# Performance work log

Hardware: AMD Instinct MI355X
Metric: run time of the kernel (lower is better)

The kernel has to match this reference:

```python
import jax, jax.numpy as jnp
import numpy as np

UNITS = 128
FILTERS = 32
KSIZE = 31
B, T, DV, DQ = 64, 1000, 512, 1024


def setup_inputs() -> dict:
    key = jax.random.key(0)
    ks = jax.random.split(key, 12)
    scale = 0.05
    inp = {
        "query": jax.random.normal(ks[0], (B, DQ), jnp.float32),
        "values": jax.random.normal(ks[1], (B, T, DV), jnp.float32),
        "previous_attention_weights": jax.random.uniform(ks[2], (B, T, 1), jnp.float32),
        # learned params
        "Wq": jax.random.normal(ks[3], (DQ, UNITS), jnp.float32) * scale,
        "bq": jnp.zeros((UNITS,), jnp.float32),
        "Wm": jax.random.normal(ks[4], (DV, UNITS), jnp.float32) * scale,
        "bm": jnp.zeros((UNITS,), jnp.float32),
        "Wv": jax.random.normal(ks[5], (UNITS, 1), jnp.float32) * scale,
        "bv": jnp.zeros((1,), jnp.float32),
        "Wconv": jax.random.normal(ks[6], (KSIZE, 1, FILTERS), jnp.float32) * scale,  # [W, Cin, Cout]
        "Wl": jax.random.normal(ks[7], (FILTERS, UNITS), jnp.float32) * scale,
    }
    return inp


def _forward(query, values, prev_w, Wq, bq, Wm, bm, Wv, bv, Wconv, Wl):
    # location features: Conv1D (same padding, no bias) then Dense(tanh, no bias)
    loc = jax.lax.conv_general_dilated(
        prev_w, Wconv, window_strides=(1,), padding="SAME",
        dimension_numbers=("NWC", "WIO", "NWC"))          # [B, T, FILTERS]
    loc = jnp.tanh(loc @ Wl)                                # [B, T, UNITS]
    q = query @ Wq + bq                                     # [B, UNITS]
    m = values @ Wm + bm                                    # [B, T, UNITS]
    score = jnp.tanh(m + q[:, None, :] + loc) @ Wv + bv     # [B, T, 1]
    attention_weights = jax.nn.softmax(score, axis=1)       # softmax over time
    context = jnp.sum(attention_weights * values, axis=1)   # [B, DV]
    return context, attention_weights


def reference(query, values, previous_attention_weights, Wq, bq, Wm, bm, Wv, bv, Wconv, Wl):
    return _forward(query, values, previous_attention_weights,
                    Wq, bq, Wm, bm, Wv, bv, Wconv, Wl)
```

## Files before the change

kernel.cpp:

```cpp
#include <hip/hip_runtime.h>

#define B_  64
#define T_  1000
#define DV_ 512
#define DQ_ 1024
#define U_  128
#define F_  32
#define KS_ 31
#define P_  8

typedef __attribute__((ext_vector_type(8))) short short8;
typedef __attribute__((ext_vector_type(4))) float f32x4;

__device__ __forceinline__ unsigned pk2(float a, float b) {
    union { float f; unsigned u; } x, y;
    x.f = a; y.f = b;
    unsigned ra = (x.u + 0x7FFFu + ((x.u >> 16) & 1u)) >> 16;
    unsigned rb = (y.u + 0x7FFFu + ((y.u >> 16) & 1u)) >> 16;
    return (ra & 0xFFFFu) | (rb << 16);
}

__device__ __forceinline__ float fast_tanh(float x) {
    return 1.0f - 2.0f / (__expf(2.0f * x) + 1.0f);
}

__device__ __forceinline__ short8 loadA8(const float* __restrict__ p) {
    float4 f0 = *(const float4*)p;
    float4 f1 = *(const float4*)(p + 4);
    int4 q;
    q.x = pk2(f0.x, f0.y); q.y = pk2(f0.z, f0.w);
    q.z = pk2(f1.x, f1.y); q.w = pk2(f1.z, f1.w);
    return *(short8*)&q;
}

__global__ void prep_kernel(const float* __restrict__ Wm, const float* __restrict__ Wl,
                            short* __restrict__ WmX, short* __restrict__ WlX) {
    int g = blockIdx.x * 256 + threadIdx.x;
    if (g < 8192) {
        int kc = g >> 9, e = g & 511;
        int n = e >> 2, q = e & 3;
        int kb = kc * 32 + q * 8;
        int4 p;
        p.x = pk2(Wm[(kb + 0) * U_ + n], Wm[(kb + 1) * U_ + n]);
        p.y = pk2(Wm[(kb + 2) * U_ + n], Wm[(kb + 3) * U_ + n]);
        p.z = pk2(Wm[(kb + 4) * U_ + n], Wm[(kb + 5) * U_ + n]);
        p.w = pk2(Wm[(kb + 6) * U_ + n], Wm[(kb + 7) * U_ + n]);
        ((int4*)WmX)[g] = p;
    } else if (g < 8704) {
        int e = g - 8192;
        int n = e >> 2, q = e & 3;
        int kb = q * 8;
        int4 p;
        p.x = pk2(Wl[(kb + 0) * U_ + n], Wl[(kb + 1) * U_ + n]);
        p.y = pk2(Wl[(kb + 2) * U_ + n], Wl[(kb + 3) * U_ + n]);
        p.z = pk2(Wl[(kb + 4) * U_ + n], Wl[(kb + 5) * U_ + n]);
        p.w = pk2(Wl[(kb + 6) * U_ + n], Wl[(kb + 7) * U_ + n]);
        ((int4*)WlX)[e] = p;
    }
}

__global__ __launch_bounds__(1024) void qb_kernel(
    const float* __restrict__ query, const float* __restrict__ Wq,
    const float* __restrict__ bq, const float* __restrict__ bm,
    float* __restrict__ qb)
{
    __shared__ float qs[DQ_];
    __shared__ float red[8][U_];
    int b = blockIdx.x, tid = threadIdx.x;
    qs[tid] = query[b * DQ_ + tid];
    __syncthreads();
    int u = tid & 127, p = tid >> 7;
    float a = 0.f;
    const float* wp = Wq + (size_t)p * 128 * U_ + u;
    const float* qp = qs + p * 128;
#pragma unroll 8
    for (int k = 0; k < 128; ++k) a += qp[k] * wp[(size_t)k * U_];
    red[p][u] = a;
    __syncthreads();
    if (tid < U_) {
        float s = bq[tid] + bm[tid];
#pragma unroll
        for (int pp = 0; pp < 8; ++pp) s += red[pp][tid];
        qb[b * U_ + tid] = s;
    }
}

__global__ __launch_bounds__(256) void score_kernel(
    const float* __restrict__ values, const float* __restrict__ prev,
    const float* __restrict__ Wc, const float* __restrict__ Wv,
    const float* __restrict__ bv, const short* __restrict__ WmX,
    const short* __restrict__ WlX, const float* __restrict__ qb,
    float* __restrict__ scores)
{
    __shared__ float WcS[KS_ * F_];
    __shared__ short AsL[2048];
    __shared__ float qbS[2 * U_];
    __shared__ float WvS[U_];

    const int tid = threadIdx.x;
    const int r0 = blockIdx.x * 64;
    const int b0 = r0 / T_;
    const int b1 = (r0 + 63) / T_;

    for (int i = tid; i < KS_ * F_; i += 256) WcS[i] = Wc[i];
    if (tid < U_) WvS[tid] = Wv[tid];
    {
        int bb = (tid < U_) ? b0 : b1;
        qbS[tid] = qb[bb * U_ + (tid & (U_ - 1))];
    }

    const int wv = tid >> 6, lane = tid & 63;
    const int quad = lane >> 4, m15 = lane & 15;
    const int row = wv * 16 + m15;
    const float* aP = values + (size_t)(r0 + row) * DV_ + quad * 8;
    const int4* bW  = (const int4*)WmX + m15 * 4 + quad;
    const int4* blW = (const int4*)WlX + m15 * 4 + quad;

    short8 afA, afB;
    int4 bfA[8], bfB[8];
    afA = loadA8(aP);
#pragma unroll
    for (int c = 0; c < 8; ++c) bfA[c] = bW[c * 64];

    __syncthreads();

    {
        int i = lane, fg = wv;
        int r = r0 + i;
        int b = r / T_;
        int t = r - b * T_;
        const float* pv = prev + b * T_;
        float a8[8] = {};
#pragma unroll
        for (int k = 0; k < KS_; ++k) {
            int tt = t + k - 15;
            float p = ((unsigned)tt < (unsigned)T_) ? pv[tt] : 0.f;
#pragma unroll
            for (int j = 0; j < 8; ++j) a8[j] += p * WcS[k * F_ + fg * 8 + j];
        }
        int4 pq;
        pq.x = pk2(a8[0], a8[1]); pq.y = pk2(a8[2], a8[3]);
        pq.z = pk2(a8[4], a8[5]); pq.w = pk2(a8[6], a8[7]);
        ((int4*)AsL)[i * 4 + (fg ^ ((i >> 1) & 3))] = pq;
    }
    __syncthreads();

    f32x4 acc[8];
    {
        short8 afl = ((const short8*)AsL)[row * 4 + (quad ^ ((row >> 1) & 3))];
        f32x4 lacc[8] = {};
#pragma unroll
        for (int c = 0; c < 8; ++c) {
            int4 bl = blW[c * 64];
            lacc[c] = __builtin_amdgcn_mfma_f32_16x16x32_bf16(afl, *(short8*)&bl, lacc[c], 0, 0, 0);
        }
        int qoff[4];
#pragma unroll
        for (int v = 0; v < 4; ++v) {
            int r = r0 + wv * 16 + quad * 4 + v;
            qoff[v] = ((r / T_) == b0) ? 0 : U_;
        }
#pragma unroll
        for (int c = 0; c < 8; ++c) {
            int col = c * 16 + m15;
#pragma unroll
            for (int v = 0; v < 4; ++v)
                acc[c][v] = qbS[qoff[v] + col] + fast_tanh(lacc[c][v]);
        }
    }

#pragma unroll
    for (int k2 = 0; k2 < 8; ++k2) {
        const int kc = k2 * 2;
        afB = loadA8(aP + (kc + 1) * 32);
#pragma unroll
        for (int c = 0; c < 8; ++c) bfB[c] = bW[(kc + 1) * 512 + c * 64];
#pragma unroll
        for (int c = 0; c < 8; ++c)
            acc[c] = __builtin_amdgcn_mfma_f32_16x16x32_bf16(afA, *(short8*)&bfA[c], acc[c], 0, 0, 0);
        if (kc + 2 < 16) {
            afA = loadA8(aP + (kc + 2) * 32);
#pragma unroll
            for (int c = 0; c < 8; ++c) bfA[c] = bW[(kc + 2) * 512 + c * 64];
        }
#pragma unroll
        for (int c = 0; c < 8; ++c)
            acc[c] = __builtin_amdgcn_mfma_f32_16x16x32_bf16(afB, *(short8*)&bfB[c], acc[c], 0, 0, 0);
    }

    float psum[4] = {0.f, 0.f, 0.f, 0.f};
#pragma unroll
    for (int c = 0; c < 8; ++c) {
        int col = c * 16 + m15;
        float wvv = WvS[col];
#pragma unroll
        for (int v = 0; v < 4; ++v)
            psum[v] += fast_tanh(acc[c][v]) * wvv;
    }
#pragma unroll
    for (int off = 1; off < 16; off <<= 1) {
#pragma unroll
        for (int v = 0; v < 4; ++v) psum[v] += __shfl_xor(psum[v], off);
    }
    if (m15 == 0) {
        float bvv = bv[0];
#pragma unroll
        for (int v = 0; v < 4; ++v)
            scores[r0 + wv * 16 + quad * 4 + v] = psum[v] + bvv;
    }
}

__global__ void softmax_kernel(const float* __restrict__ s, float* __restrict__ w) {
    __shared__ float red[4];
    int b = blockIdx.x, tid = threadIdx.x;
    const float* sb = s + b * T_;
    float v[4];
    int tv[4];
#pragma unroll
    for (int i = 0; i < 4; ++i) {
        int t = tid + i * 256;
        tv[i] = t;
        v[i] = (t < T_) ? sb[t] : -1e30f;
    }
    float mx = fmaxf(fmaxf(v[0], v[1]), fmaxf(v[2], v[3]));
#pragma unroll
    for (int off = 32; off >= 1; off >>= 1) mx = fmaxf(mx, __shfl_xor(mx, off));
    int wv = tid >> 6, lane = tid & 63;
    if (lane == 0) red[wv] = mx;
    __syncthreads();
    mx = fmaxf(fmaxf(red[0], red[1]), fmaxf(red[2], red[3]));
    float e[4];
    float sum = 0.f;
#pragma unroll
    for (int i = 0; i < 4; ++i) {
        e[i] = (tv[i] < T_) ? __expf(v[i] - mx) : 0.f;
        sum += e[i];
    }
#pragma unroll
    for (int off = 32; off >= 1; off >>= 1) sum += __shfl_xor(sum, off);
    __syncthreads();
    if (lane == 0) red[wv] = sum;
    __syncthreads();
    sum = red[0] + red[1] + red[2] + red[3];
    float inv = 1.0f / sum;
#pragma unroll
    for (int i = 0; i < 4; ++i)
        if (tv[i] < T_) w[b * T_ + tv[i]] = e[i] * inv;
}

__global__ __launch_bounds__(256) void ctx1_kernel(
    const float* __restrict__ values, const float* __restrict__ w,
    float* __restrict__ part)
{
    __shared__ float wS[125];
    int b = blockIdx.x, p = blockIdx.y, tid = threadIdx.x;
    if (tid < 125) wS[tid] = w[b * T_ + p * 125 + tid];
    __syncthreads();
    const float* vp = values + ((size_t)b * T_ + p * 125) * DV_ + tid * 2;
    float ax = 0.f, ay = 0.f;
#pragma unroll 5
    for (int t = 0; t < 125; ++t) {
        float2 v = *(const float2*)(vp + (size_t)t * DV_);
        ax += wS[t] * v.x;
        ay += wS[t] * v.y;
    }
    float2 o; o.x = ax; o.y = ay;
    *(float2*)(part + ((size_t)(b * P_ + p)) * DV_ + tid * 2) = o;
}

__global__ void ctx2_kernel(const float* __restrict__ part, float* __restrict__ ctx) {
    int b = blockIdx.x, tid = threadIdx.x;
    float ax = 0.f, ay = 0.f;
    const float* pp = part + (size_t)b * P_ * DV_ + tid * 2;
#pragma unroll
    for (int p = 0; p < P_; ++p) {
        float2 v = *(const float2*)(pp + (size_t)p * DV_);
        ax += v.x; ay += v.y;
    }
    float2 o; o.x = ax; o.y = ay;
    *(float2*)(ctx + (size_t)b * DV_ + tid * 2) = o;
}

extern "C" void kernel_launch(void* const* d_in, const int* in_sizes, int n_in,
                              void* d_out, int out_size, void* d_ws, size_t ws_size,
                              hipStream_t stream) {
    const float* query  = (const float*)d_in[0];
    const float* values = (const float*)d_in[1];
    const float* prev   = (const float*)d_in[2];
    const float* Wq     = (const float*)d_in[3];
    const float* bq     = (const float*)d_in[4];
    const float* Wm     = (const float*)d_in[5];
    const float* bm     = (const float*)d_in[6];
    const float* Wv     = (const float*)d_in[7];
    const float* bv     = (const float*)d_in[8];
    const float* Wc     = (const float*)d_in[9];
    const float* Wl     = (const float*)d_in[10];

    float* out  = (float*)d_out;
    float* ctx  = out;
    float* attw = out + B_ * DV_;

    char* ws = (char*)d_ws;
    float* qb     = (float*)(ws);
    float* scores = (float*)(ws + 32768);
    short* WmX    = (short*)(ws + 32768 + 256000);
    short* WlX    = (short*)(ws + 32768 + 256000 + 131072);
    float* part   = (float*)(ws + 32768 + 256000 + 131072 + 8192);

    prep_kernel<<<34, 256, 0, stream>>>(Wm, Wl, WmX, WlX);
    qb_kernel<<<B_, 1024, 0, stream>>>(query, Wq, bq, bm, qb);
    score_kernel<<<1000, 256, 0, stream>>>(values, prev, Wc, Wv, bv, WmX, WlX, qb, scores);
    softmax_kernel<<<B_, 256, 0, stream>>>(scores, attw);
    ctx1_kernel<<<dim3(B_, P_), 256, 0, stream>>>(values, attw, part);
    ctx2_kernel<<<B_, 256, 0, stream>>>(part, ctx);
}
```

Measured before the change: 273.6 us.

## Merge prep and qb kernels, double score tile rows, widen ctx partitions

Prep and qb kernels are merged into one launch. The score kernel now processes 128 rows per block with two MFMA row groups sharing each weight fragment, which halves the B-operand traffic per row, and it uses a three-stage register prefetch of activations. The context reduction is split into 16 time chunks using float4 loads and an in-block two-way reduction, and ctx2 is vectorized. These changes raise register pressure in the score kernel and leave only 500 blocks to fill the device.

```diff
diff --git a/kernel.cpp b/kernel.cpp
--- a/kernel.cpp
+++ b/kernel.cpp
@@ -7,7 +7,8 @@
 #define U_  128
 #define F_  32
 #define KS_ 31
-#define P_  8
+#define P_  16
+#define CT_ 63
 
 typedef __attribute__((ext_vector_type(8))) short short8;
 typedef __attribute__((ext_vector_type(4))) float f32x4;
@@ -24,64 +25,64 @@
     return 1.0f - 2.0f / (__expf(2.0f * x) + 1.0f);
 }
 
-__device__ __forceinline__ short8 loadA8(const float* __restrict__ p) {
-    float4 f0 = *(const float4*)p;
-    float4 f1 = *(const float4*)(p + 4);
+__device__ __forceinline__ short8 pk8(float4 f0, float4 f1) {
     int4 q;
     q.x = pk2(f0.x, f0.y); q.y = pk2(f0.z, f0.w);
     q.z = pk2(f1.x, f1.y); q.w = pk2(f1.z, f1.w);
     return *(short8*)&q;
 }
 
-__global__ void prep_kernel(const float* __restrict__ Wm, const float* __restrict__ Wl,
-                            short* __restrict__ WmX, short* __restrict__ WlX) {
-    int g = blockIdx.x * 256 + threadIdx.x;
-    if (g < 8192) {
-        int kc = g >> 9, e = g & 511;
-        int n = e >> 2, q = e & 3;
-        int kb = kc * 32 + q * 8;
-        int4 p;
-        p.x = pk2(Wm[(kb + 0) * U_ + n], Wm[(kb + 1) * U_ + n]);
-        p.y = pk2(Wm[(kb + 2) * U_ + n], Wm[(kb + 3) * U_ + n]);
-        p.z = pk2(Wm[(kb + 4) * U_ + n], Wm[(kb + 5) * U_ + n]);
-        p.w = pk2(Wm[(kb + 6) * U_ + n], Wm[(kb + 7) * U_ + n]);
-        ((int4*)WmX)[g] = p;
-    } else if (g < 8704) {
-        int e = g - 8192;
-        int n = e >> 2, q = e & 3;
-        int kb = q * 8;
-        int4 p;
-        p.x = pk2(Wl[(kb + 0) * U_ + n], Wl[(kb + 1) * U_ + n]);
-        p.y = pk2(Wl[(kb + 2) * U_ + n], Wl[(kb + 3) * U_ + n]);
-        p.z = pk2(Wl[(kb + 4) * U_ + n], Wl[(kb + 5) * U_ + n]);
-        p.w = pk2(Wl[(kb + 6) * U_ + n], Wl[(kb + 7) * U_ + n]);
-        ((int4*)WlX)[e] = p;
-    }
-}
-
-__global__ __launch_bounds__(1024) void qb_kernel(
+__global__ __launch_bounds__(1024) void prep_qb_kernel(
+    const float* __restrict__ Wm, const float* __restrict__ Wl,
     const float* __restrict__ query, const float* __restrict__ Wq,
     const float* __restrict__ bq, const float* __restrict__ bm,
-    float* __restrict__ qb)
+    short* __restrict__ WmX, short* __restrict__ WlX, float* __restrict__ qb)
 {
-    __shared__ float qs[DQ_];
-    __shared__ float red[8][U_];
-    int b = blockIdx.x, tid = threadIdx.x;
-    qs[tid] = query[b * DQ_ + tid];
-    __syncthreads();
-    int u = tid & 127, p = tid >> 7;
-    float a = 0.f;
-    const float* wp = Wq + (size_t)p * 128 * U_ + u;
-    const float* qp = qs + p * 128;
+    __shared__ float sh[DQ_ + 8 * U_];
+    int blk = blockIdx.x, tid = threadIdx.x;
+    if (blk < 9) {
+        int g = blk * 1024 + tid;
+        if (g < 8192) {
+            int kc = g >> 9, e = g & 511;
+            int n = e >> 2, q = e & 3;
+            int kb = kc * 32 + q * 8;
+            int4 p;
+            p.x = pk2(Wm[(kb + 0) * U_ + n], Wm[(kb + 1) * U_ + n]);
+            p.y = pk2(Wm[(kb + 2) * U_ + n], Wm[(kb + 3) * U_ + n]);
+            p.z = pk2(Wm[(kb + 4) * U_ + n], Wm[(kb + 5) * U_ + n]);
+            p.w = pk2(Wm[(kb + 6) * U_ + n], Wm[(kb + 7) * U_ + n]);
+            ((int4*)WmX)[g] = p;
+        } else if (g < 8704) {
+            int e = g - 8192;
+            int n = e >> 2, q = e & 3;
+            int kb = q * 8;
+            int4 p;
+            p.x = pk2(Wl[(kb + 0) * U_ + n], Wl[(kb + 1) * U_ + n]);
+            p.y = pk2(Wl[(kb + 2) * U_ + n], Wl[(kb + 3) * U_ + n]);
+            p.z = pk2(Wl[(kb + 4) * U_ + n], Wl[(kb + 5) * U_ + n]);
+            p.w = pk2(Wl[(kb + 6) * U_ + n], Wl[(kb + 7) * U_ + n]);
+            ((int4*)WlX)[e] = p;
+        }
+    } else {
+        float* qs = sh;
+        float* red = sh + DQ_;
+        int b = blk - 9;
+        qs[tid] = query[b * DQ_ + tid];
+        __syncthreads();
+        int u = tid & 127, p = tid >> 7;
+        float a = 0.f;
+        const float* wp = Wq + (size_t)p * 128 * U_ + u;
+        const float* qp = qs + p * 128;
 #pragma unroll 8
-    for (int k = 0; k < 128; ++k) a += qp[k] * wp[(size_t)k * U_];
-    red[p][u] = a;
-    __syncthreads();
-    if (tid < U_) {
-        float s = bq[tid] + bm[tid];
-#pragma unroll
-        for (int pp = 0; pp < 8; ++pp) s += red[pp][tid];
-        qb[b * U_ + tid] = s;
+        for (int k = 0; k < 128; ++k) a += qp[k] * wp[(size_t)k * U_];
+        red[p * U_ + u] = a;
+        __syncthreads();
+        if (tid < U_) {
+            float s = bq[tid] + bm[tid];
+#pragma unroll
+            for (int pp = 0; pp < 8; ++pp) s += red[pp * U_ + tid];
+            qb[b * U_ + tid] = s;
+        }
     }
 }
 
@@ -93,14 +94,14 @@
     float* __restrict__ scores)
 {
     __shared__ float WcS[KS_ * F_];
-    __shared__ short AsL[2048];
+    __shared__ short AsL[128 * 32];
     __shared__ float qbS[2 * U_];
     __shared__ float WvS[U_];
 
     const int tid = threadIdx.x;
-    const int r0 = blockIdx.x * 64;
+    const int r0 = blockIdx.x * 128;
     const int b0 = r0 / T_;
-    const int b1 = (r0 + 63) / T_;
+    const int b1 = (r0 + 127) / T_;
 
     for (int i = tid; i < KS_ * F_; i += 256) WcS[i] = Wc[i];
     if (tid < U_) WvS[tid] = Wv[tid];
@@ -111,21 +112,27 @@
 
     const int wv = tid >> 6, lane = tid & 63;
     const int quad = lane >> 4, m15 = lane & 15;
-    const int row = wv * 16 + m15;
-    const float* aP = values + (size_t)(r0 + row) * DV_ + quad * 8;
+    const int row0 = wv * 32 + m15;
+    const float* aP0 = values + (size_t)(r0 + row0) * DV_ + quad * 8;
+    const float* aP1 = aP0 + (size_t)16 * DV_;
     const int4* bW  = (const int4*)WmX + m15 * 4 + quad;
     const int4* blW = (const int4*)WlX + m15 * 4 + quad;
 
-    short8 afA, afB;
-    int4 bfA[8], bfB[8];
-    afA = loadA8(aP);
-#pragma unroll
-    for (int c = 0; c < 8; ++c) bfA[c] = bW[c * 64];
-
-    __syncthreads();
-
-    {
-        int i = lane, fg = wv;
+    float4 aq0[2][2], aq1[2][2], aq2[2][2];
+    int4 bf0[8], bf1[8];
+    aq0[0][0] = *(const float4*)(aP0);      aq0[0][1] = *(const float4*)(aP0 + 4);
+    aq0[1][0] = *(const float4*)(aP1);      aq0[1][1] = *(const float4*)(aP1 + 4);
+    aq1[0][0] = *(const float4*)(aP0 + 32); aq1[0][1] = *(const float4*)(aP0 + 36);
+    aq1[1][0] = *(const float4*)(aP1 + 32); aq1[1][1] = *(const float4*)(aP1 + 36);
+#pragma unroll
+    for (int c = 0; c < 8; ++c) bf0[c] = bW[c * 64];
+
+    __syncthreads();
+
+#pragma unroll
+    for (int it = 0; it < 2; ++it) {
+        int idx = tid + it * 256;
+        int i = idx & 127, fg = idx >> 7;
         int r = r0 + i;
         int b = r / T_;
         int t = r - b * T_;
@@ -145,68 +152,89 @@
     }
     __syncthreads();
 
-    f32x4 acc[8];
+    f32x4 acc[2][8] = {};
     {
-        short8 afl = ((const short8*)AsL)[row * 4 + (quad ^ ((row >> 1) & 3))];
-        f32x4 lacc[8] = {};
+        int row1 = row0 + 16;
+        short8 afl0 = ((const short8*)AsL)[row0 * 4 + (quad ^ ((row0 >> 1) & 3))];
+        short8 afl1 = ((const short8*)AsL)[row1 * 4 + (quad ^ ((row1 >> 1) & 3))];
 #pragma unroll
         for (int c = 0; c < 8; ++c) {
             int4 bl = blW[c * 64];
-            lacc[c] = __builtin_amdgcn_mfma_f32_16x16x32_bf16(afl, *(short8*)&bl, lacc[c], 0, 0, 0);
-        }
-        int qoff[4];
-#pragma unroll
-        for (int v = 0; v < 4; ++v) {
-            int r = r0 + wv * 16 + quad * 4 + v;
-            qoff[v] = ((r / T_) == b0) ? 0 : U_;
-        }
+            acc[0][c] = __builtin_amdgcn_mfma_f32_16x16x32_bf16(afl0, *(short8*)&bl, acc[0][c], 0, 0, 0);
+            acc[1][c] = __builtin_amdgcn_mfma_f32_16x16x32_bf16(afl1, *(short8*)&bl, acc[1][c], 0, 0, 0);
+        }
+        int qoff[2][4];
+#pragma unroll
+        for (int g = 0; g < 2; ++g)
+#pragma unroll
+            for (int v = 0; v < 4; ++v) {
+                int r = r0 + wv * 32 + g * 16 + quad * 4 + v;
+                qoff[g][v] = ((r / T_) == b0) ? 0 : U_;
+            }
+#pragma unroll
+        for (int g = 0; g < 2; ++g)
+#pragma unroll
+            for (int c = 0; c < 8; ++c) {
+                int col = c * 16 + m15;
+#pragma unroll
+                for (int v = 0; v < 4; ++v)
+                    acc[g][c][v] = qbS[qoff[g][v] + col] + fast_tanh(acc[g][c][v]);
+            }
+    }
+
+#pragma unroll
+    for (int kc = 0; kc < 16; ++kc) {
+        if (kc + 2 < 16) {
+            aq2[0][0] = *(const float4*)(aP0 + (kc + 2) * 32);
+            aq2[0][1] = *(const float4*)(aP0 + (kc + 2) * 32 + 4);
+            aq2[1][0] = *(const float4*)(aP1 + (kc + 2) * 32);
+            aq2[1][1] = *(const float4*)(aP1 + (kc + 2) * 32 + 4);
+        }
+        if (kc + 1 < 16) {
+#pragma unroll
+            for (int c = 0; c < 8; ++c) bf1[c] = bW[(kc + 1) * 512 + c * 64];
+        }
+        short8 af0 = pk8(aq0[0][0], aq0[0][1]);
+        short8 af1 = pk8(aq0[1][0], aq0[1][1]);
+#pragma unroll
+        for (int c = 0; c < 8; ++c) {
+            acc[0][c] = __builtin_amdgcn_mfma_f32_16x16x32_bf16(af0, *(short8*)&bf0[c], acc[0][c], 0, 0, 0);
+            acc[1][c] = __builtin_amdgcn_mfma_f32_16x16x32_bf16(af1, *(short8*)&bf0[c], acc[1][c], 0, 0, 0);
+        }
+#pragma unroll
+        for (int g = 0; g < 2; ++g) {
+            aq0[g][0] = aq1[g][0]; aq0[g][1] = aq1[g][1];
+            aq1[g][0] = aq2[g][0]; aq1[g][1] = aq2[g][1];
+        }
+#pragma unroll
+        for (int c = 0; c < 8; ++c) bf0[c] = bf1[c];
+    }
+
+    float psum[2][4] = {};
+#pragma unroll
+    for (int g = 0; g < 2; ++g)
 #pragma unroll
         for (int c = 0; c < 8; ++c) {
             int col = c * 16 + m15;
+            float wvv = WvS[col];
 #pragma unroll
             for (int v = 0; v < 4; ++v)
-                acc[c][v] = qbS[qoff[v] + col] + fast_tanh(lacc[c][v]);
-        }
-    }
-
-#pragma unroll
-    for (int k2 = 0; k2 < 8; ++k2) {
-        const int kc = k2 * 2;
-        afB = loadA8(aP + (kc + 1) * 32);
-#pragma unroll
-        for (int c = 0; c < 8; ++c) bfB[c] = bW[(kc + 1) * 512 + c * 64];
-#pragma unroll
-        for (int c = 0; c < 8; ++c)
-            acc[c] = __builtin_amdgcn_mfma_f32_16x16x32_bf16(afA, *(short8*)&bfA[c], acc[c], 0, 0, 0);
-        if (kc + 2 < 16) {
-            afA = loadA8(aP + (kc + 2) * 32);
-#pragma unroll
-            for (int c = 0; c < 8; ++c) bfA[c] = bW[(kc + 2) * 512 + c * 64];
-        }
-#pragma unroll
-        for (int c = 0; c < 8; ++c)
-            acc[c] = __builtin_amdgcn_mfma_f32_16x16x32_bf16(afB, *(short8*)&bfB[c], acc[c], 0, 0, 0);
-    }
-
-    float psum[4] = {0.f, 0.f, 0.f, 0.f};
-#pragma unroll
-    for (int c = 0; c < 8; ++c) {
-        int col = c * 16 + m15;
-        float wvv = WvS[col];
-#pragma unroll
-        for (int v = 0; v < 4; ++v)
-            psum[v] += fast_tanh(acc[c][v]) * wvv;
-    }
+                psum[g][v] += fast_tanh(acc[g][c][v]) * wvv;
+        }
 #pragma unroll
     for (int off = 1; off < 16; off <<= 1) {
 #pragma unroll
-        for (int v = 0; v < 4; ++v) psum[v] += __shfl_xor(psum[v], off);
+        for (int g = 0; g < 2; ++g)
+#pragma unroll
+            for (int v = 0; v < 4; ++v) psum[g][v] += __shfl_xor(psum[g][v], off);
     }
     if (m15 == 0) {
         float bvv = bv[0];
 #pragma unroll
-        for (int v = 0; v < 4; ++v)
-            scores[r0 + wv * 16 + quad * 4 + v] = psum[v] + bvv;
+        for (int g = 0; g < 2; ++g)
+#pragma unroll
+            for (int v = 0; v < 4; ++v)
+                scores[r0 + wv * 32 + g * 16 + quad * 4 + v] = psum[g][v] + bvv;
     }
 }
 
@@ -252,33 +280,41 @@
     const float* __restrict__ values, const float* __restrict__ w,
     float* __restrict__ part)
 {
-    __shared__ float wS[125];
+    __shared__ float wS[CT_];
+    __shared__ float4 ps[128];
     int b = blockIdx.x, p = blockIdx.y, tid = threadIdx.x;
-    if (tid < 125) wS[tid] = w[b * T_ + p * 125 + tid];
-    __syncthreads();
-    const float* vp = values + ((size_t)b * T_ + p * 125) * DV_ + tid * 2;
-    float ax = 0.f, ay = 0.f;
-#pragma unroll 5
-    for (int t = 0; t < 125; ++t) {
-        float2 v = *(const float2*)(vp + (size_t)t * DV_);
-        ax += wS[t] * v.x;
-        ay += wS[t] * v.y;
-    }
-    float2 o; o.x = ax; o.y = ay;
-    *(float2*)(part + ((size_t)(b * P_ + p)) * DV_ + tid * 2) = o;
+    int t0 = p * CT_;
+    int len = (T_ - t0 < CT_) ? (T_ - t0) : CT_;
+    if (tid < len) wS[tid] = w[b * T_ + t0 + tid];
+    __syncthreads();
+    int cl = tid & 127, tp = tid >> 7;
+    const float* vp = values + ((size_t)b * T_ + t0) * DV_ + cl * 4;
+    float4 a = {0.f, 0.f, 0.f, 0.f};
+#pragma unroll 4
+    for (int t = tp; t < len; t += 2) {
+        float4 v = *(const float4*)(vp + (size_t)t * DV_);
+        float wt = wS[t];
+        a.x += wt * v.x; a.y += wt * v.y; a.z += wt * v.z; a.w += wt * v.w;
+    }
+    if (tp == 1) ps[cl] = a;
+    __syncthreads();
+    if (tp == 0) {
+        float4 o = ps[cl];
+        o.x += a.x; o.y += a.y; o.z += a.z; o.w += a.w;
+        *(float4*)(part + ((size_t)(b * P_ + p)) * DV_ + cl * 4) = o;
+    }
 }
 
 __global__ void ctx2_kernel(const float* __restrict__ part, float* __restrict__ ctx) {
     int b = blockIdx.x, tid = threadIdx.x;
-    float ax = 0.f, ay = 0.f;
-    const float* pp = part + (size_t)b * P_ * DV_ + tid * 2;
+    const float* pp = part + (size_t)b * P_ * DV_ + tid * 4;
+    float4 s = {0.f, 0.f, 0.f, 0.f};
 #pragma unroll
     for (int p = 0; p < P_; ++p) {
-        float2 v = *(const float2*)(pp + (size_t)p * DV_);
-        ax += v.x; ay += v.y;
-    }
-    float2 o; o.x = ax; o.y = ay;
-    *(float2*)(ctx + (size_t)b * DV_ + tid * 2) = o;
+        float4 v = *(const float4*)(pp + (size_t)p * DV_);
+        s.x += v.x; s.y += v.y; s.z += v.z; s.w += v.w;
+    }
+    *(float4*)(ctx + (size_t)b * DV_ + tid * 4) = s;
 }
 
 extern "C" void kernel_launch(void* const* d_in, const int* in_sizes, int n_in,
@@ -303,14 +339,13 @@
     char* ws = (char*)d_ws;
     float* qb     = (float*)(ws);
     float* scores = (float*)(ws + 32768);
-    short* WmX    = (short*)(ws + 32768 + 256000);
-    short* WlX    = (short*)(ws + 32768 + 256000 + 131072);
-    float* part   = (float*)(ws + 32768 + 256000 + 131072 + 8192);
-
-    prep_kernel<<<34, 256, 0, stream>>>(Wm, Wl, WmX, WlX);
-    qb_kernel<<<B_, 1024, 0, stream>>>(query, Wq, bq, bm, qb);
-    score_kernel<<<1000, 256, 0, stream>>>(values, prev, Wc, Wv, bv, WmX, WlX, qb, scores);
+    short* WmX    = (short*)(ws + 288768);
+    short* WlX    = (short*)(ws + 419840);
+    float* part   = (float*)(ws + 428032);
+
+    prep_qb_kernel<<<73, 1024, 0, stream>>>(Wm, Wl, query, Wq, bq, bm, WmX, WlX, qb);
+    score_kernel<<<500, 256, 0, stream>>>(values, prev, Wc, Wv, bv, WmX, WlX, qb, scores);
     softmax_kernel<<<B_, 256, 0, stream>>>(scores, attw);
     ctx1_kernel<<<dim3(B_, P_), 256, 0, stream>>>(values, attw, part);
-    ctx2_kernel<<<B_, 256, 0, stream>>>(part, ctx);
-}
+    ctx2_kernel<<<B_, 128, 0, stream>>>(part, ctx);
+}
```

New measurement: 272.8 us. Within noise of the previous version (-0.3%).
